# Optimization experiments

Measured on AMD Instinct MI355X. Metric: run time of the kernel, lower is better.

Reference implementation:

```python
import jax, jax.numpy as jnp
import numpy as np

N = 50000
E = 800000
IN_DIM = 128
EMB_DIM = 64
HID = 128
OUT_DIM = 64
VOCAB = 1000
NUM_GRAPHS = 128


def _gat(x, src, dst, W, a_s, a_d, b, n):
    # PyG GATConv, heads=1: h = x @ W (no bias); alpha_e = leaky_relu(a_s.h_src + a_d.h_dst, 0.2)
    h = x @ W                                  # [n, C]
    as_n = h @ a_s                             # [n]
    ad_n = h @ a_d                             # [n]
    logit = jax.nn.leaky_relu(as_n[src] + ad_n[dst], negative_slope=0.2)  # [E']
    # segment softmax over destination node
    m = jax.ops.segment_max(logit, dst, num_segments=n)
    e = jnp.exp(logit - m[dst])
    s = jax.ops.segment_sum(e, dst, num_segments=n)
    coef = e / s[dst]                          # [E']
    out = jax.ops.segment_sum(h[src] * coef[:, None], dst, num_segments=n)
    return out + b


def setup_inputs() -> dict:
    key = jax.random.key(0)
    ks = jax.random.split(key, 20)
    inp = {
        "x": jax.random.normal(ks[0], (N, IN_DIM), dtype=jnp.float32),
        "node_index": jax.random.randint(ks[1], (N,), 0, VOCAB),
        "edge_index": jax.random.randint(ks[2], (2, E), 0, N),
        "batch": jnp.sort(jax.random.randint(ks[3], (N,), 0, NUM_GRAPHS)),
        "emb": jax.random.normal(ks[4], (VOCAB, EMB_DIM), dtype=jnp.float32) * 0.1,
        "W1": jax.random.normal(ks[5], (IN_DIM + EMB_DIM, HID), dtype=jnp.float32) * 0.05,
        "a1s": jax.random.normal(ks[6], (HID,), dtype=jnp.float32) * 0.1,
        "a1d": jax.random.normal(ks[7], (HID,), dtype=jnp.float32) * 0.1,
        "b1": jnp.zeros((HID,), dtype=jnp.float32),
        "W2": jax.random.normal(ks[8], (HID, HID), dtype=jnp.float32) * 0.05,
        "a2s": jax.random.normal(ks[9], (HID,), dtype=jnp.float32) * 0.1,
        "a2d": jax.random.normal(ks[10], (HID,), dtype=jnp.float32) * 0.1,
        "b2": jnp.zeros((HID,), dtype=jnp.float32),
        "W3": jax.random.normal(ks[11], (HID, HID), dtype=jnp.float32) * 0.05,
        "a3s": jax.random.normal(ks[12], (HID,), dtype=jnp.float32) * 0.1,
        "a3d": jax.random.normal(ks[13], (HID,), dtype=jnp.float32) * 0.1,
        "b3": jnp.zeros((HID,), dtype=jnp.float32),
        "fcW": jax.random.normal(ks[14], (HID, OUT_DIM), dtype=jnp.float32) * 0.05,
        "fcb": jnp.zeros((OUT_DIM,), dtype=jnp.float32),
    }
    return inp


def reference(x, node_index, edge_index, batch, emb, W1, a1s, a1d, b1,
              W2, a2s, a2d, b2, W3, a3s, a3d, b3, fcW, fcb):
    n = x.shape[0]
    # embedding lookup + L2 normalize features, then concat
    ev = emb[node_index]                       # [N, EMB_DIM]
    norms = jnp.linalg.norm(x, axis=1, keepdims=True)
    norms = jnp.where(norms == 0, 1e-8, norms)
    h = jnp.concatenate([x / norms, ev], axis=1)  # [N, IN+EMB]
    # add self loops (PyG GATConv default add_self_loops=True)
    loop = jnp.arange(n)
    src = jnp.concatenate([edge_index[0], loop])
    dst = jnp.concatenate([edge_index[1], loop])
    h = jax.nn.gelu(_gat(h, src, dst, W1, a1s, a1d, b1, n))
    h = jax.nn.gelu(_gat(h, src, dst, W2, a2s, a2d, b2, n))
    h = jax.nn.gelu(_gat(h, src, dst, W3, a3s, a3d, b3, n))
    # global_add_pool over graphs
    g = jax.ops.segment_sum(h, batch, num_segments=NUM_GRAPHS)  # [G, HID]
    out = g @ fcW + fcb
    return jax.nn.leaky_relu(out, negative_slope=0.01)
```

## Files before the change

kernel.cpp:

```cpp
#include <hip/hip_runtime.h>

#define N_NODES 50000
#define N_EDGES 800000
#define IN_DIM 128
#define EMB_DIM 64
#define HID 128
#define OUT_DIM 64
#define NUM_GRAPHS 128
#define E_TOT (N_EDGES + N_NODES)
#define K1 (IN_DIM + EMB_DIM)
#define NB 391
#define EPT 16
#define EPB (256 * EPT)

typedef __attribute__((ext_vector_type(8))) short bf16x8;
typedef __attribute__((ext_vector_type(4))) float f32x4;

__device__ __forceinline__ float gelu_f(float x) {
    float x3 = x * x * x;
    return 0.5f * x * (1.0f + tanhf(0.7978845608028654f * (x + 0.044715f * x3)));
}
__device__ __forceinline__ float lrelu02(float x) { return x > 0.f ? x : 0.2f * x; }
__device__ __forceinline__ float rl_f(float v, int j) {
    return __int_as_float(__builtin_amdgcn_readlane(__float_as_int(v), j));
}
__device__ __forceinline__ unsigned short f2bf(float f) {
    unsigned u = __float_as_uint(f);
    unsigned r = (u + 0x7fffu + ((u >> 16) & 1u)) >> 16;
    return (unsigned short)r;
}
__device__ __forceinline__ unsigned pk2bf(float a, float b) {
    return (unsigned)f2bf(a) | ((unsigned)f2bf(b) << 16);
}

__global__ __launch_bounds__(256) void k_zero(int* __restrict__ bcnt, int* __restrict__ bfill) {
    int t = blockIdx.x * 256 + threadIdx.x;
    if (t < NB) { bcnt[t] = 0; bfill[t] = 0; }
}

__global__ __launch_bounds__(128) void k_prepW3(const float* __restrict__ W1, unsigned short* __restrict__ Wt1,
                                                const float* __restrict__ W2, unsigned short* __restrict__ Wt2,
                                                const float* __restrict__ W3, unsigned short* __restrict__ Wt3) {
    int b = blockIdx.x;
    int c = threadIdx.x;
    if (b < K1) {
        Wt1[(size_t)c * (K1 + 8) + b] = f2bf(W1[(size_t)b * HID + c]);
    } else if (b < K1 + HID) {
        int k = b - K1;
        Wt2[(size_t)c * (HID + 8) + k] = f2bf(W2[(size_t)k * HID + c]);
    } else {
        int k = b - K1 - HID;
        Wt3[(size_t)c * (HID + 8) + k] = f2bf(W3[(size_t)k * HID + c]);
    }
}

__global__ __launch_bounds__(256) void k_prepA(const float* __restrict__ x, const int* __restrict__ nidx,
                                               const float* __restrict__ emb, unsigned* __restrict__ Abu) {
    int lane = threadIdx.x & 63;
    int node = (blockIdx.x * 256 + threadIdx.x) >> 6;
    if (node >= N_NODES) return;
    float2 v = ((const float2*)(x + (size_t)node * IN_DIM))[lane];
    float ss = v.x * v.x + v.y * v.y;
#pragma unroll
    for (int o = 32; o; o >>= 1) ss += __shfl_xor(ss, o);
    float nrm = sqrtf(ss);
    if (nrm == 0.f) nrm = 1e-8f;
    float inv = 1.f / nrm;
    unsigned* row = Abu + (size_t)node * (K1 / 2);
    row[lane] = pk2bf(v.x * inv, v.y * inv);
    int nid = __builtin_amdgcn_readfirstlane(nidx[node]);
    if (lane < 32) {
        float2 e = ((const float2*)(emb + (size_t)nid * EMB_DIM))[lane];
        row[64 + lane] = pk2bf(e.x, e.y);
    }
}

__global__ __launch_bounds__(256) void k_bhist(const int* __restrict__ dst, int* __restrict__ bcnt) {
    __shared__ int h[NB];
    for (int i = threadIdx.x; i < NB; i += 256) h[i] = 0;
    __syncthreads();
    for (int e = blockIdx.x * 256 + threadIdx.x; e < N_EDGES; e += gridDim.x * 256)
        atomicAdd(&h[dst[e] >> 7], 1);
    __syncthreads();
    for (int i = threadIdx.x; i < NB; i += 256)
        if (h[i]) atomicAdd(&bcnt[i], h[i]);
}

__global__ __launch_bounds__(512) void k_bscan(const int* __restrict__ bcnt, int* __restrict__ boff,
                                               int* __restrict__ rowptr) {
    __shared__ int sh[512];
    int t = threadIdx.x;
    int v = (t < NB) ? bcnt[t] : 0;
    sh[t] = v;
    __syncthreads();
    for (int o = 1; o < 512; o <<= 1) {
        int u = (t >= o) ? sh[t - o] : 0;
        __syncthreads();
        sh[t] += u;
        __syncthreads();
    }
    if (t < NB) boff[t] = sh[t] - v;
    if (t == NB - 1) boff[NB] = sh[t];
    if (t == 0) rowptr[N_NODES] = E_TOT;
}

__global__ __launch_bounds__(256) void k_passA(const int* __restrict__ src, const int* __restrict__ dst,
                                               const int* __restrict__ boff, int* __restrict__ bfill,
                                               unsigned* __restrict__ barr) {
    __shared__ int h[NB];
    __shared__ int base[NB];
    for (int i = threadIdx.x; i < NB; i += 256) h[i] = 0;
    __syncthreads();
    int e0 = blockIdx.x * EPB;
    int tag[EPT];
#pragma unroll
    for (int i = 0; i < EPT; i++) {
        int e = e0 + i * 256 + threadIdx.x;
        tag[i] = -1;
        if (e < N_EDGES) {
            int b = dst[e] >> 7;
            int r = atomicAdd(&h[b], 1);
            tag[i] = (b << 12) | r;
        }
    }
    __syncthreads();
    for (int i = threadIdx.x; i < NB; i += 256)
        base[i] = h[i] ? atomicAdd(&bfill[i], h[i]) : 0;
    __syncthreads();
#pragma unroll
    for (int i = 0; i < EPT; i++) {
        if (tag[i] >= 0) {
            int e = e0 + i * 256 + threadIdx.x;
            int b = tag[i] >> 12, r = tag[i] & 0xfff;
            unsigned s = (unsigned)src[e];
            unsigned dl = (unsigned)(dst[e] & 127);
            barr[boff[b] + base[b] + r] = s | (dl << 16);
        }
    }
}

__global__ __launch_bounds__(256) void k_passB(const unsigned* __restrict__ barr, const int* __restrict__ boff,
                                               int* __restrict__ rowptr, int* __restrict__ csr) {
    __shared__ int dcnt[128];
    __shared__ int dsum[128];
    __shared__ int locOff[128];
    int b = blockIdx.x;
    int t = threadIdx.x;
    int n0 = b << 7;
    int cnt = min(128, N_NODES - n0);
    int eb = boff[b], ee = boff[b + 1];
    if (t < 128) dcnt[t] = 0;
    __syncthreads();
    for (int i = eb + t; i < ee; i += 256) atomicAdd(&dcnt[barr[i] >> 16], 1);
    __syncthreads();
    int v = 0;
    if (t < 128) {
        v = (t < cnt) ? dcnt[t] + 1 : 0;
        dsum[t] = v;
    }
    __syncthreads();
    for (int o = 1; o < 128; o <<= 1) {
        int u = (t >= o && t < 128) ? dsum[t - o] : 0;
        __syncthreads();
        if (t < 128) dsum[t] += u;
        __syncthreads();
    }
    int csrBase = eb + n0;
    if (t < 128) {
        locOff[t] = dsum[t] - v;
        dcnt[t] = 0;
    }
    if (t < cnt) {
        int loc = dsum[t] - v;
        rowptr[n0 + t] = csrBase + loc;
        csr[csrBase + loc] = n0 + t;
    }
    __syncthreads();
    for (int i = eb + t; i < ee; i += 256) {
        unsigned vv = barr[i];
        int dl = vv >> 16;
        int s = (int)(vv & 0xffffu);
        int k = atomicAdd(&dcnt[dl], 1);
        csr[csrBase + locOff[dl] + 1 + k] = s;
    }
}

template <int K>
__global__ __launch_bounds__(256) void k_mgemm(const unsigned short* __restrict__ Abf,
                                               const unsigned short* __restrict__ WtP,
                                               const float* __restrict__ a_s, const float* __restrict__ a_d,
                                               unsigned short* __restrict__ Hbf,
                                               float* __restrict__ asn, float* __restrict__ adn) {
    constexpr int KP = K + 8;
    constexpr int NK = K / 32;
    __shared__ __align__(16) unsigned short Wl[128 * KP];
    {
        const uint4* gsrc = (const uint4*)WtP;
        uint4* ldst = (uint4*)Wl;
        const int nchunk = 128 * KP * 2 / 16;
        for (int i = threadIdx.x; i < nchunk; i += 256) ldst[i] = gsrc[i];
    }
    int lane = threadIdx.x & 63;
    int wv = threadIdx.x >> 6;
    int rowbase = blockIdx.x * 64 + wv * 16;
    if (rowbase >= N_NODES) { __syncthreads(); return; }
    int l15 = lane & 15, quad = lane >> 4;

    const unsigned short* Abase = Abf + (size_t)(rowbase + l15) * K + quad * 8;
    bf16x8 afr[NK];
#pragma unroll
    for (int i = 0; i < NK; i++) afr[i] = *(const bf16x8*)(Abase + i * 32);

    __syncthreads();

    f32x4 acc[8];
#pragma unroll
    for (int t = 0; t < 8; t++) acc[t] = (f32x4){0.f, 0.f, 0.f, 0.f};
#pragma unroll
    for (int i = 0; i < NK; i++) {
#pragma unroll
        for (int t = 0; t < 8; t++) {
            bf16x8 bf = *(const bf16x8*)(&Wl[(t * 16 + l15) * KP + i * 32 + quad * 8]);
            acc[t] = __builtin_amdgcn_mfma_f32_16x16x32_bf16(afr[i], bf, acc[t], 0, 0, 0);
        }
    }
    float asc[8], adc[8];
#pragma unroll
    for (int t = 0; t < 8; t++) { asc[t] = a_s[t * 16 + l15]; adc[t] = a_d[t * 16 + l15]; }
#pragma unroll
    for (int r = 0; r < 4; r++) {
        int row = rowbase + quad * 4 + r;
        float ps = 0.f, pd = 0.f;
#pragma unroll
        for (int t = 0; t < 8; t++) {
            float v = acc[t][r];
            Hbf[(size_t)row * HID + t * 16 + l15] = f2bf(v);
            ps = fmaf(v, asc[t], ps);
            pd = fmaf(v, adc[t], pd);
        }
#pragma unroll
        for (int o = 1; o < 16; o <<= 1) {
            ps += __shfl_xor(ps, o);
            pd += __shfl_xor(pd, o);
        }
        if (l15 == 0) { asn[row] = ps; adn[row] = pd; }
    }
}

template <bool OUT32>
__global__ __launch_bounds__(256) void k_aggr(const int* __restrict__ rowptr, const int* __restrict__ csr,
                                              const float* __restrict__ asn, const float* __restrict__ adn,
                                              const unsigned short* __restrict__ hbf,
                                              const float* __restrict__ bias, void* __restrict__ outp) {
    __shared__ float sh_e[4][64];
    __shared__ int sh_s[4][64];
    int lane = threadIdx.x & 63;
    int w = threadIdx.x >> 6;
    int node = blockIdx.x * 4 + w;
    if (node >= N_NODES) return;
    int st = rowptr[node], en = rowptr[node + 1];
    int deg = en - st;
    float ad = adn[node];
    const unsigned* hu = (const unsigned*)hbf;
    float2 acc = make_float2(0.f, 0.f);

    if (deg <= 64) {
        int s = 0;
        float l = -1e30f;
        if (lane < deg) {
            s = csr[st + lane];
            l = lrelu02(asn[s] + ad);
        }
        float m = l;
#pragma unroll
        for (int o = 32; o; o >>= 1) m = fmaxf(m, __shfl_xor(m, o));
        float e = (lane < deg) ? __expf(l - m) : 0.f;
        float ssum = e;
#pragma unroll
        for (int o = 32; o; o >>= 1) ssum += __shfl_xor(ssum, o);
        float coef = e / ssum;
        int j = 0;
        for (; j + 8 <= deg; j += 8) {
            int si[8];
            float ci[8];
            unsigned vi[8];
#pragma unroll
            for (int q = 0; q < 8; q++) {
                si[q] = __builtin_amdgcn_readlane(s, j + q);
                ci[q] = rl_f(coef, j + q);
            }
#pragma unroll
            for (int q = 0; q < 8; q++) vi[q] = hu[(size_t)si[q] * 64 + lane];
#pragma unroll
            for (int q = 0; q < 8; q++) {
                acc.x = fmaf(ci[q], __int_as_float(vi[q] << 16), acc.x);
                acc.y = fmaf(ci[q], __int_as_float(vi[q] & 0xffff0000u), acc.y);
            }
        }
        for (; j + 4 <= deg; j += 4) {
            int s0 = __builtin_amdgcn_readlane(s, j);
            int s1 = __builtin_amdgcn_readlane(s, j + 1);
            int s2 = __builtin_amdgcn_readlane(s, j + 2);
            int s3 = __builtin_amdgcn_readlane(s, j + 3);
            float c0 = rl_f(coef, j), c1 = rl_f(coef, j + 1);
            float c2 = rl_f(coef, j + 2), c3 = rl_f(coef, j + 3);
            unsigned v0 = hu[(size_t)s0 * 64 + lane];
            unsigned v1 = hu[(size_t)s1 * 64 + lane];
            unsigned v2 = hu[(size_t)s2 * 64 + lane];
            unsigned v3 = hu[(size_t)s3 * 64 + lane];
            acc.x = fmaf(c0, __int_as_float(v0 << 16), acc.x);
            acc.y = fmaf(c0, __int_as_float(v0 & 0xffff0000u), acc.y);
            acc.x = fmaf(c1, __int_as_float(v1 << 16), acc.x);
            acc.y = fmaf(c1, __int_as_float(v1 & 0xffff0000u), acc.y);
            acc.x = fmaf(c2, __int_as_float(v2 << 16), acc.x);
            acc.y = fmaf(c2, __int_as_float(v2 & 0xffff0000u), acc.y);
            acc.x = fmaf(c3, __int_as_float(v3 << 16), acc.x);
            acc.y = fmaf(c3, __int_as_float(v3 & 0xffff0000u), acc.y);
        }
        for (; j < deg; j++) {
            int s0 = __builtin_amdgcn_readlane(s, j);
            float c0 = rl_f(coef, j);
            unsigned v0 = hu[(size_t)s0 * 64 + lane];
            acc.x = fmaf(c0, __int_as_float(v0 << 16), acc.x);
            acc.y = fmaf(c0, __int_as_float(v0 & 0xffff0000u), acc.y);
        }
    } else {
        float m = -1e30f;
        for (int i = st + lane; i < en; i += 64) {
            float l = lrelu02(asn[csr[i]] + ad);
            m = fmaxf(m, l);
        }
#pragma unroll
        for (int o = 32; o; o >>= 1) m = fmaxf(m, __shfl_xor(m, o));
        float ssum = 0.f;
        for (int i = st + lane; i < en; i += 64) {
            float l = lrelu02(asn[csr[i]] + ad);
            ssum += __expf(l - m);
        }
#pragma unroll
        for (int o = 32; o; o >>= 1) ssum += __shfl_xor(ssum, o);
        float inv = 1.f / ssum;
        for (int base = st; base < en; base += 64) {
            int cnt = min(64, en - base);
            if (lane < cnt) {
                int sx = csr[base + lane];
                float l = lrelu02(asn[sx] + ad);
                sh_e[w][lane] = __expf(l - m) * inv;
                sh_s[w][lane] = sx;
            }
            for (int j = 0; j < cnt; j++) {
                float c = sh_e[w][j];
                int sx = sh_s[w][j];
                unsigned v0 = hu[(size_t)sx * 64 + lane];
                acc.x = fmaf(c, __int_as_float(v0 << 16), acc.x);
                acc.y = fmaf(c, __int_as_float(v0 & 0xffff0000u), acc.y);
            }
        }
    }
    float2 b = ((const float2*)bias)[lane];
    float rx = gelu_f(acc.x + b.x);
    float ry = gelu_f(acc.y + b.y);
    if constexpr (OUT32) {
        ((float2*)outp)[(size_t)node * 64 + lane] = make_float2(rx, ry);
    } else {
        ((unsigned*)outp)[(size_t)node * 64 + lane] = pk2bf(rx, ry);
    }
}

__global__ __launch_bounds__(256) void k_poolfc(const float* __restrict__ h, const int* __restrict__ batch,
                                                const float* __restrict__ fcW, const float* __restrict__ fcb,
                                                float* __restrict__ out) {
    __shared__ float gv[HID];
    __shared__ float tmp[256];
    int g = blockIdx.x;
    int st, en;
    {
        int lo = 0, hi = N_NODES;
        while (lo < hi) { int mid = (lo + hi) >> 1; if (batch[mid] < g) lo = mid + 1; else hi = mid; }
        st = lo;
        lo = st; hi = N_NODES;
        while (lo < hi) { int mid = (lo + hi) >> 1; if (batch[mid] < g + 1) lo = mid + 1; else hi = mid; }
        en = lo;
    }
    int c = threadIdx.x & 127;
    int half = threadIdx.x >> 7;
    float acc = 0.f;
#pragma unroll 4
    for (int n = st + half; n < en; n += 2) acc += h[(size_t)n * HID + c];
    tmp[threadIdx.x] = acc;
    __syncthreads();
    if (threadIdx.x < HID) gv[threadIdx.x] = tmp[threadIdx.x] + tmp[threadIdx.x + 128];
    __syncthreads();
    if (threadIdx.x < OUT_DIM) {
        float a = fcb[threadIdx.x];
#pragma unroll 4
        for (int k = 0; k < HID; k++) a = fmaf(gv[k], fcW[k * OUT_DIM + threadIdx.x], a);
        out[g * OUT_DIM + threadIdx.x] = a > 0.f ? a : 0.01f * a;
    }
}

extern "C" void kernel_launch(void* const* d_in, const int* in_sizes, int n_in,
                              void* d_out, int out_size, void* d_ws, size_t ws_size,
                              hipStream_t stream) {
    const float* x    = (const float*)d_in[0];
    const int* nidx   = (const int*)d_in[1];
    const int* ei     = (const int*)d_in[2];
    const int* batch  = (const int*)d_in[3];
    const float* emb  = (const float*)d_in[4];
    const float* W1   = (const float*)d_in[5];
    const float* a1s  = (const float*)d_in[6];
    const float* a1d  = (const float*)d_in[7];
    const float* b1   = (const float*)d_in[8];
    const float* W2   = (const float*)d_in[9];
    const float* a2s  = (const float*)d_in[10];
    const float* a2d  = (const float*)d_in[11];
    const float* b2   = (const float*)d_in[12];
    const float* W3   = (const float*)d_in[13];
    const float* a3s  = (const float*)d_in[14];
    const float* a3d  = (const float*)d_in[15];
    const float* b3   = (const float*)d_in[16];
    const float* fcW  = (const float*)d_in[17];
    const float* fcb  = (const float*)d_in[18];
    float* out = (float*)d_out;
    const int* srcA = ei;
    const int* dstA = ei + N_EDGES;

    char* w = (char*)d_ws;
    auto alloc = [&](size_t bytes) -> char* {
        char* p = w;
        w += (bytes + 511) & ~(size_t)511;
        return p;
    };
    char* region0 = alloc((size_t)N_NODES * HID * 4);
    unsigned* Abu = (unsigned*)region0;
    float* h3f    = (float*)region0;
    unsigned short* hLin = (unsigned short*)alloc((size_t)N_NODES * HID * 2);
    unsigned short* hAct = (unsigned short*)alloc((size_t)N_NODES * HID * 2);
    float* asn   = (float*)alloc((size_t)N_NODES * 4);
    float* adn   = (float*)alloc((size_t)N_NODES * 4);
    int* rowptr  = (int*)alloc((size_t)(N_NODES + 1) * 4);
    int* bcnt    = (int*)alloc((size_t)NB * 4);
    int* boff    = (int*)alloc((size_t)(NB + 1) * 4);
    int* bfill   = (int*)alloc((size_t)NB * 4);
    unsigned* barr = (unsigned*)alloc((size_t)N_EDGES * 4);
    int* csr     = (int*)alloc((size_t)E_TOT * 4);
    unsigned short* Wt1 = (unsigned short*)alloc((size_t)HID * (K1 + 8) * 2);
    unsigned short* Wt2 = (unsigned short*)alloc((size_t)HID * (HID + 8) * 2);
    unsigned short* Wt3 = (unsigned short*)alloc((size_t)HID * (HID + 8) * 2);

    k_zero<<<(NB + 255) / 256, 256, 0, stream>>>(bcnt, bfill);
    k_prepW3<<<K1 + 2 * HID, 128, 0, stream>>>(W1, Wt1, W2, Wt2, W3, Wt3);
    k_prepA<<<(N_NODES + 3) / 4, 256, 0, stream>>>(x, nidx, emb, Abu);

    k_bhist<<<512, 256, 0, stream>>>(dstA, bcnt);
    k_bscan<<<1, 512, 0, stream>>>(bcnt, boff, rowptr);
    k_passA<<<(N_EDGES + EPB - 1) / EPB, 256, 0, stream>>>(srcA, dstA, boff, bfill, barr);
    k_passB<<<NB, 256, 0, stream>>>(barr, boff, rowptr, csr);

    int gemmBlocks = (N_NODES + 63) / 64;
    int aggrBlocks = (N_NODES + 3) / 4;

    k_mgemm<K1><<<gemmBlocks, 256, 0, stream>>>((const unsigned short*)Abu, Wt1, a1s, a1d, hLin, asn, adn);
    k_aggr<false><<<aggrBlocks, 256, 0, stream>>>(rowptr, csr, asn, adn, hLin, b1, hAct);
    k_mgemm<HID><<<gemmBlocks, 256, 0, stream>>>(hAct, Wt2, a2s, a2d, hLin, asn, adn);
    k_aggr<false><<<aggrBlocks, 256, 0, stream>>>(rowptr, csr, asn, adn, hLin, b2, hAct);
    k_mgemm<HID><<<gemmBlocks, 256, 0, stream>>>(hAct, Wt3, a3s, a3d, hLin, asn, adn);
    k_aggr<true><<<aggrBlocks, 256, 0, stream>>>(rowptr, csr, asn, adn, hLin, b3, h3f);

    k_poolfc<<<NUM_GRAPHS, 256, 0, stream>>>(h3f, batch, fcW, fcb, out);
}
```

Measured before the change: 334.3 us.

## Fuse all stages into one cooperative persistent kernel with grid syncs

Replaces the sequence of about thirteen kernel launches with a single cooperative persistent kernel whose grid-stride phases are separated by grid.sync(), and keeps a multi-launch fallback. The GEMM phase no longer stages the weight matrix in shared memory and instead reads bf16 weight fragments straight from global memory, and the weight transposes drop their padding. The aim is to remove launch gaps and tail effects between the many small phases. In exchange, the persistent grid is capped by occupancy at 4 blocks per CU under the launch bounds, the grid-wide barriers add their own cost, and uncached weight loads may slow the GEMMs.

```diff
diff --git a/kernel.cpp b/kernel.cpp
--- a/kernel.cpp
+++ b/kernel.cpp
@@ -1,4 +1,6 @@
 #include <hip/hip_runtime.h>
+#include <hip/hip_cooperative_groups.h>
+namespace cg = cooperative_groups;
 
 #define N_NODES 50000
 #define N_EDGES 800000
@@ -10,8 +12,11 @@
 #define E_TOT (N_EDGES + N_NODES)
 #define K1 (IN_DIM + EMB_DIM)
 #define NB 391
+#define EPB 4096
+#define NCHUNK ((N_EDGES + EPB - 1) / EPB)
 #define EPT 16
-#define EPB (256 * EPT)
+#define NGRP 12500
+#define NRG 782
 
 typedef __attribute__((ext_vector_type(8))) short bf16x8;
 typedef __attribute__((ext_vector_type(4))) float f32x4;
@@ -33,397 +38,443 @@
     return (unsigned)f2bf(a) | ((unsigned)f2bf(b) << 16);
 }
 
-__global__ __launch_bounds__(256) void k_zero(int* __restrict__ bcnt, int* __restrict__ bfill) {
-    int t = blockIdx.x * 256 + threadIdx.x;
-    if (t < NB) { bcnt[t] = 0; bfill[t] = 0; }
-}
-
-__global__ __launch_bounds__(128) void k_prepW3(const float* __restrict__ W1, unsigned short* __restrict__ Wt1,
-                                                const float* __restrict__ W2, unsigned short* __restrict__ Wt2,
-                                                const float* __restrict__ W3, unsigned short* __restrict__ Wt3) {
-    int b = blockIdx.x;
-    int c = threadIdx.x;
-    if (b < K1) {
-        Wt1[(size_t)c * (K1 + 8) + b] = f2bf(W1[(size_t)b * HID + c]);
-    } else if (b < K1 + HID) {
-        int k = b - K1;
-        Wt2[(size_t)c * (HID + 8) + k] = f2bf(W2[(size_t)k * HID + c]);
-    } else {
-        int k = b - K1 - HID;
-        Wt3[(size_t)c * (HID + 8) + k] = f2bf(W3[(size_t)k * HID + c]);
-    }
-}
-
-__global__ __launch_bounds__(256) void k_prepA(const float* __restrict__ x, const int* __restrict__ nidx,
-                                               const float* __restrict__ emb, unsigned* __restrict__ Abu) {
-    int lane = threadIdx.x & 63;
-    int node = (blockIdx.x * 256 + threadIdx.x) >> 6;
-    if (node >= N_NODES) return;
-    float2 v = ((const float2*)(x + (size_t)node * IN_DIM))[lane];
-    float ss = v.x * v.x + v.y * v.y;
-#pragma unroll
-    for (int o = 32; o; o >>= 1) ss += __shfl_xor(ss, o);
-    float nrm = sqrtf(ss);
-    if (nrm == 0.f) nrm = 1e-8f;
-    float inv = 1.f / nrm;
-    unsigned* row = Abu + (size_t)node * (K1 / 2);
-    row[lane] = pk2bf(v.x * inv, v.y * inv);
-    int nid = __builtin_amdgcn_readfirstlane(nidx[node]);
-    if (lane < 32) {
-        float2 e = ((const float2*)(emb + (size_t)nid * EMB_DIM))[lane];
-        row[64 + lane] = pk2bf(e.x, e.y);
-    }
-}
-
-__global__ __launch_bounds__(256) void k_bhist(const int* __restrict__ dst, int* __restrict__ bcnt) {
+struct MegaArgs {
+    const float* x; const int* nidx; const int* src; const int* dst; const int* batch;
+    const float* emb;
+    const float* W1; const float* a1s; const float* a1d; const float* b1;
+    const float* W2; const float* a2s; const float* a2d; const float* b2;
+    const float* W3; const float* a3s; const float* a3d; const float* b3;
+    const float* fcW; const float* fcb;
+    float* out;
+    unsigned* Abu; float* h3f;
+    unsigned short* hLin; unsigned short* hAct;
+    float* asn; float* adn;
+    int* rowptr; int* bcnt; int* boff; int* bfill;
+    unsigned* barr; int* csr;
+    unsigned short* Wt1; unsigned short* Wt2; unsigned short* Wt3;
+};
+
+
+__device__ void phase_p0(const MegaArgs& A) {
+    const int tid = threadIdx.x, bid = blockIdx.x;
+    const int lane = tid & 63, wv = tid >> 6;
+    const int gtid = bid * 256 + tid;
+    const int nthr = gridDim.x * 256;
+    for (int i = gtid; i < NB; i += nthr) { A.bcnt[i] = 0; A.bfill[i] = 0; }
+    for (int id = gtid; id < 128 * K1; id += nthr) {
+        int c = id / K1, k = id - c * K1;
+        A.Wt1[c * K1 + k] = f2bf(A.W1[(size_t)k * HID + c]);
+    }
+    for (int id = gtid; id < 128 * 128; id += nthr) {
+        int c = id >> 7, k = id & 127;
+        A.Wt2[c * HID + k] = f2bf(A.W2[(size_t)k * HID + c]);
+        A.Wt3[c * HID + k] = f2bf(A.W3[(size_t)k * HID + c]);
+    }
+    for (int g4 = bid; g4 < NGRP; g4 += gridDim.x) {
+        int node = g4 * 4 + wv;
+        if (node >= N_NODES) continue;
+        float2 v = ((const float2*)(A.x + (size_t)node * IN_DIM))[lane];
+        float ss = v.x * v.x + v.y * v.y;
+#pragma unroll
+        for (int o = 32; o; o >>= 1) ss += __shfl_xor(ss, o);
+        float nrm = sqrtf(ss);
+        if (nrm == 0.f) nrm = 1e-8f;
+        float inv = 1.f / nrm;
+        unsigned* row = A.Abu + (size_t)node * (K1 / 2);
+        row[lane] = pk2bf(v.x * inv, v.y * inv);
+        int nid = __builtin_amdgcn_readfirstlane(A.nidx[node]);
+        if (lane < 32) {
+            float2 e = ((const float2*)(A.emb + (size_t)nid * EMB_DIM))[lane];
+            row[64 + lane] = pk2bf(e.x, e.y);
+        }
+    }
+}
+
+__device__ void phase_bhist(const MegaArgs& A, int* h) {
+    const int tid = threadIdx.x;
+    for (int c = blockIdx.x; c < NCHUNK; c += gridDim.x) {
+        for (int i = tid; i < NB; i += 256) h[i] = 0;
+        __syncthreads();
+        int e0 = c * EPB, e1 = min(e0 + EPB, N_EDGES);
+        for (int e = e0 + tid; e < e1; e += 256) atomicAdd(&h[A.dst[e] >> 7], 1);
+        __syncthreads();
+        for (int i = tid; i < NB; i += 256)
+            if (h[i]) atomicAdd(&A.bcnt[i], h[i]);
+        __syncthreads();
+    }
+}
+
+__device__ void phase_bscan(const MegaArgs& A) {
+    const int tid = threadIdx.x;
+    const int lane = tid & 63;
+    if (blockIdx.x == 0 && (tid >> 6) == 0) {
+        int run = 0;
+        for (int c = 0; c < 7; c++) {
+            int i = c * 64 + lane;
+            int v = (i < NB) ? A.bcnt[i] : 0;
+            int s = v;
+#pragma unroll
+            for (int o = 1; o < 64; o <<= 1) {
+                int u = __shfl_up(s, o);
+                if (lane >= o) s += u;
+            }
+            if (i < NB) A.boff[i] = run + s - v;
+            run += __shfl(s, 63);
+        }
+        if (lane == 0) { A.boff[NB] = N_EDGES; A.rowptr[N_NODES] = E_TOT; }
+    }
+}
+
+__device__ void phase_passA(const MegaArgs& A, int* h, int* base) {
+    const int tid = threadIdx.x;
+    for (int c = blockIdx.x; c < NCHUNK; c += gridDim.x) {
+        for (int i = tid; i < NB; i += 256) h[i] = 0;
+        __syncthreads();
+        int e0 = c * EPB;
+        int tag[EPT];
+#pragma unroll
+        for (int i = 0; i < EPT; i++) {
+            int e = e0 + i * 256 + tid;
+            tag[i] = -1;
+            if (e < N_EDGES) {
+                int b = A.dst[e] >> 7;
+                int r = atomicAdd(&h[b], 1);
+                tag[i] = (b << 12) | r;
+            }
+        }
+        __syncthreads();
+        for (int i = tid; i < NB; i += 256)
+            base[i] = h[i] ? atomicAdd(&A.bfill[i], h[i]) : 0;
+        __syncthreads();
+#pragma unroll
+        for (int i = 0; i < EPT; i++) {
+            if (tag[i] >= 0) {
+                int e = e0 + i * 256 + tid;
+                int b = tag[i] >> 12, r = tag[i] & 0xfff;
+                A.barr[A.boff[b] + base[b] + r] =
+                    (unsigned)A.src[e] | ((unsigned)(A.dst[e] & 127) << 16);
+            }
+        }
+        __syncthreads();
+    }
+}
+
+__device__ void phase_passB(const MegaArgs& A, int* dcnt, int* dsum, int* locOff) {
+    const int tid = threadIdx.x;
+    for (int b = blockIdx.x; b < NB; b += gridDim.x) {
+        int n0 = b << 7;
+        int cnt = min(128, N_NODES - n0);
+        int eb = A.boff[b], ee = A.boff[b + 1];
+        if (tid < 128) dcnt[tid] = 0;
+        __syncthreads();
+        for (int i = eb + tid; i < ee; i += 256) atomicAdd(&dcnt[A.barr[i] >> 16], 1);
+        __syncthreads();
+        int v = 0;
+        if (tid < 128) {
+            v = (tid < cnt) ? dcnt[tid] + 1 : 0;
+            dsum[tid] = v;
+        }
+        __syncthreads();
+        for (int o = 1; o < 128; o <<= 1) {
+            int u = (tid >= o && tid < 128) ? dsum[tid - o] : 0;
+            __syncthreads();
+            if (tid < 128) dsum[tid] += u;
+            __syncthreads();
+        }
+        int csrBase = eb + n0;
+        if (tid < 128) {
+            locOff[tid] = dsum[tid] - v;
+            dcnt[tid] = 0;
+        }
+        if (tid < cnt) {
+            int loc = dsum[tid] - v;
+            A.rowptr[n0 + tid] = csrBase + loc;
+            A.csr[csrBase + loc] = n0 + tid;
+        }
+        __syncthreads();
+        for (int i = eb + tid; i < ee; i += 256) {
+            unsigned vv = A.barr[i];
+            int dl = vv >> 16;
+            int s = (int)(vv & 0xffffu);
+            int k = atomicAdd(&dcnt[dl], 1);
+            A.csr[csrBase + locOff[dl] + 1 + k] = s;
+        }
+        __syncthreads();
+    }
+}
+
+template <int K>
+__device__ void phase_mgemm(const unsigned short* __restrict__ Abf, const unsigned short* __restrict__ Wt,
+                            const float* __restrict__ a_s, const float* __restrict__ a_d,
+                            unsigned short* __restrict__ Hbf, float* __restrict__ asn,
+                            float* __restrict__ adn) {
+    const int lane = threadIdx.x & 63;
+    const int wv = threadIdx.x >> 6;
+    const int l15 = lane & 15, quad = lane >> 4;
+    constexpr int NK = K / 32;
+    for (int rg = blockIdx.x; rg < NRG; rg += gridDim.x) {
+        int rowbase = rg * 64 + wv * 16;
+        if (rowbase >= N_NODES) continue;
+        const unsigned short* Abase = Abf + (size_t)(rowbase + l15) * K + quad * 8;
+        bf16x8 afr[NK];
+#pragma unroll
+        for (int i = 0; i < NK; i++) afr[i] = *(const bf16x8*)(Abase + i * 32);
+        f32x4 acc[8];
+#pragma unroll
+        for (int t = 0; t < 8; t++) acc[t] = (f32x4){0.f, 0.f, 0.f, 0.f};
+#pragma unroll
+        for (int i = 0; i < NK; i++) {
+#pragma unroll
+            for (int t = 0; t < 8; t++) {
+                bf16x8 bf = *(const bf16x8*)(Wt + (size_t)(t * 16 + l15) * K + i * 32 + quad * 8);
+                acc[t] = __builtin_amdgcn_mfma_f32_16x16x32_bf16(afr[i], bf, acc[t], 0, 0, 0);
+            }
+        }
+        float asc[8], adc[8];
+#pragma unroll
+        for (int t = 0; t < 8; t++) { asc[t] = a_s[t * 16 + l15]; adc[t] = a_d[t * 16 + l15]; }
+#pragma unroll
+        for (int r = 0; r < 4; r++) {
+            int row = rowbase + quad * 4 + r;
+            float ps = 0.f, pd = 0.f;
+#pragma unroll
+            for (int t = 0; t < 8; t++) {
+                float v = acc[t][r];
+                Hbf[(size_t)row * HID + t * 16 + l15] = f2bf(v);
+                ps = fmaf(v, asc[t], ps);
+                pd = fmaf(v, adc[t], pd);
+            }
+#pragma unroll
+            for (int o = 1; o < 16; o <<= 1) {
+                ps += __shfl_xor(ps, o);
+                pd += __shfl_xor(pd, o);
+            }
+            if (l15 == 0) { asn[row] = ps; adn[row] = pd; }
+        }
+    }
+}
+
+template <bool OUT32>
+__device__ void phase_aggr(const MegaArgs& A, const unsigned short* __restrict__ hbf,
+                           const float* __restrict__ bias, void* __restrict__ outp, char* smem) {
+    float* sh_e = (float*)smem;
+    int* sh_s = (int*)(smem + 1024);
+    const int lane = threadIdx.x & 63;
+    const int w = threadIdx.x >> 6;
+    const unsigned* hu = (const unsigned*)hbf;
+    const int* rowptr = A.rowptr;
+    const int* csr = A.csr;
+    const float* asn = A.asn;
+    const float* adn = A.adn;
+    for (int ng = blockIdx.x; ng < NGRP; ng += gridDim.x) {
+        int node = ng * 4 + w;
+        if (node >= N_NODES) continue;
+        int st = rowptr[node], en = rowptr[node + 1];
+        int deg = en - st;
+        float ad = adn[node];
+        float2 acc = make_float2(0.f, 0.f);
+        if (deg <= 64) {
+            int s = 0;
+            float l = -1e30f;
+            if (lane < deg) {
+                s = csr[st + lane];
+                l = lrelu02(asn[s] + ad);
+            }
+            float m = l;
+#pragma unroll
+            for (int o = 32; o; o >>= 1) m = fmaxf(m, __shfl_xor(m, o));
+            float e = (lane < deg) ? __expf(l - m) : 0.f;
+            float ssum = e;
+#pragma unroll
+            for (int o = 32; o; o >>= 1) ssum += __shfl_xor(ssum, o);
+            float coef = e / ssum;
+            int j = 0;
+            for (; j + 8 <= deg; j += 8) {
+                int si[8]; float ci[8]; unsigned vi[8];
+#pragma unroll
+                for (int q = 0; q < 8; q++) {
+                    si[q] = __builtin_amdgcn_readlane(s, j + q);
+                    ci[q] = rl_f(coef, j + q);
+                }
+#pragma unroll
+                for (int q = 0; q < 8; q++) vi[q] = hu[(size_t)si[q] * 64 + lane];
+#pragma unroll
+                for (int q = 0; q < 8; q++) {
+                    acc.x = fmaf(ci[q], __int_as_float(vi[q] << 16), acc.x);
+                    acc.y = fmaf(ci[q], __int_as_float(vi[q] & 0xffff0000u), acc.y);
+                }
+            }
+            for (; j < deg; j++) {
+                int s0 = __builtin_amdgcn_readlane(s, j);
+                float c0 = rl_f(coef, j);
+                unsigned v0 = hu[(size_t)s0 * 64 + lane];
+                acc.x = fmaf(c0, __int_as_float(v0 << 16), acc.x);
+                acc.y = fmaf(c0, __int_as_float(v0 & 0xffff0000u), acc.y);
+            }
+        } else {
+            float m = -1e30f;
+            for (int i = st + lane; i < en; i += 64) {
+                float l = lrelu02(asn[csr[i]] + ad);
+                m = fmaxf(m, l);
+            }
+#pragma unroll
+            for (int o = 32; o; o >>= 1) m = fmaxf(m, __shfl_xor(m, o));
+            float ssum = 0.f;
+            for (int i = st + lane; i < en; i += 64) {
+                float l = lrelu02(asn[csr[i]] + ad);
+                ssum += __expf(l - m);
+            }
+#pragma unroll
+            for (int o = 32; o; o >>= 1) ssum += __shfl_xor(ssum, o);
+            float inv = 1.f / ssum;
+            for (int base = st; base < en; base += 64) {
+                int cnt = min(64, en - base);
+                if (lane < cnt) {
+                    int sx = csr[base + lane];
+                    float l = lrelu02(asn[sx] + ad);
+                    sh_e[w * 64 + lane] = __expf(l - m) * inv;
+                    sh_s[w * 64 + lane] = sx;
+                }
+                for (int j = 0; j < cnt; j++) {
+                    float c = sh_e[w * 64 + j];
+                    int sx = sh_s[w * 64 + j];
+                    unsigned v0 = hu[(size_t)sx * 64 + lane];
+                    acc.x = fmaf(c, __int_as_float(v0 << 16), acc.x);
+                    acc.y = fmaf(c, __int_as_float(v0 & 0xffff0000u), acc.y);
+                }
+            }
+        }
+        float2 b = ((const float2*)bias)[lane];
+        float rx = gelu_f(acc.x + b.x);
+        float ry = gelu_f(acc.y + b.y);
+        if constexpr (OUT32) {
+            ((float2*)outp)[(size_t)node * 64 + lane] = make_float2(rx, ry);
+        } else {
+            ((unsigned*)outp)[(size_t)node * 64 + lane] = pk2bf(rx, ry);
+        }
+    }
+}
+
+__device__ void phase_poolfc(const MegaArgs& A, char* smem) {
+    float* gv = (float*)smem;
+    float* tmp = (float*)(smem + 512);
+    const int tid = threadIdx.x;
+    for (int g = blockIdx.x; g < NUM_GRAPHS; g += gridDim.x) {
+        int st, en;
+        {
+            int lo = 0, hi = N_NODES;
+            while (lo < hi) { int mid = (lo + hi) >> 1; if (A.batch[mid] < g) lo = mid + 1; else hi = mid; }
+            st = lo;
+            lo = st; hi = N_NODES;
+            while (lo < hi) { int mid = (lo + hi) >> 1; if (A.batch[mid] < g + 1) lo = mid + 1; else hi = mid; }
+            en = lo;
+        }
+        int c = tid & 127;
+        int half = tid >> 7;
+        float acc = 0.f;
+        for (int n = st + half; n < en; n += 2) acc += A.h3f[(size_t)n * HID + c];
+        tmp[tid] = acc;
+        __syncthreads();
+        if (tid < HID) gv[tid] = tmp[tid] + tmp[tid + 128];
+        __syncthreads();
+        if (tid < OUT_DIM) {
+            float a = A.fcb[tid];
+#pragma unroll 4
+            for (int k = 0; k < HID; k++) a = fmaf(gv[k], A.fcW[k * OUT_DIM + tid], a);
+            A.out[g * OUT_DIM + tid] = a > 0.f ? a : 0.01f * a;
+        }
+        __syncthreads();
+    }
+}
+
+__global__ __launch_bounds__(256, 4) void k_mega(MegaArgs A) {
+    __shared__ __align__(16) char smem[4608];
+    cg::grid_group grid = cg::this_grid();
+    phase_p0(A);
+    grid.sync();
+    phase_bhist(A, (int*)smem);
+    grid.sync();
+    phase_bscan(A);
+    grid.sync();
+    phase_passA(A, (int*)smem, (int*)(smem + 1568));
+    grid.sync();
+    phase_passB(A, (int*)smem, (int*)(smem + 512), (int*)(smem + 1024));
+    grid.sync();
+    phase_mgemm<K1>((const unsigned short*)A.Abu, A.Wt1, A.a1s, A.a1d, A.hLin, A.asn, A.adn);
+    grid.sync();
+    phase_aggr<false>(A, A.hLin, A.b1, A.hAct, smem);
+    grid.sync();
+    phase_mgemm<HID>(A.hAct, A.Wt2, A.a2s, A.a2d, A.hLin, A.asn, A.adn);
+    grid.sync();
+    phase_aggr<false>(A, A.hLin, A.b2, A.hAct, smem);
+    grid.sync();
+    phase_mgemm<HID>(A.hAct, A.Wt3, A.a3s, A.a3d, A.hLin, A.asn, A.adn);
+    grid.sync();
+    phase_aggr<true>(A, A.hLin, A.b3, A.h3f, smem);
+    grid.sync();
+    phase_poolfc(A, smem);
+}
+
+__global__ __launch_bounds__(256) void kf_p0(MegaArgs A) { phase_p0(A); }
+__global__ __launch_bounds__(256) void kf_bhist(MegaArgs A) {
     __shared__ int h[NB];
-    for (int i = threadIdx.x; i < NB; i += 256) h[i] = 0;
-    __syncthreads();
-    for (int e = blockIdx.x * 256 + threadIdx.x; e < N_EDGES; e += gridDim.x * 256)
-        atomicAdd(&h[dst[e] >> 7], 1);
-    __syncthreads();
-    for (int i = threadIdx.x; i < NB; i += 256)
-        if (h[i]) atomicAdd(&bcnt[i], h[i]);
-}
-
-__global__ __launch_bounds__(512) void k_bscan(const int* __restrict__ bcnt, int* __restrict__ boff,
-                                               int* __restrict__ rowptr) {
-    __shared__ int sh[512];
-    int t = threadIdx.x;
-    int v = (t < NB) ? bcnt[t] : 0;
-    sh[t] = v;
-    __syncthreads();
-    for (int o = 1; o < 512; o <<= 1) {
-        int u = (t >= o) ? sh[t - o] : 0;
-        __syncthreads();
-        sh[t] += u;
-        __syncthreads();
-    }
-    if (t < NB) boff[t] = sh[t] - v;
-    if (t == NB - 1) boff[NB] = sh[t];
-    if (t == 0) rowptr[N_NODES] = E_TOT;
-}
-
-__global__ __launch_bounds__(256) void k_passA(const int* __restrict__ src, const int* __restrict__ dst,
-                                               const int* __restrict__ boff, int* __restrict__ bfill,
-                                               unsigned* __restrict__ barr) {
+    phase_bhist(A, h);
+}
+__global__ __launch_bounds__(256) void kf_bscan(MegaArgs A) { phase_bscan(A); }
+__global__ __launch_bounds__(256) void kf_passA(MegaArgs A) {
     __shared__ int h[NB];
     __shared__ int base[NB];
-    for (int i = threadIdx.x; i < NB; i += 256) h[i] = 0;
-    __syncthreads();
-    int e0 = blockIdx.x * EPB;
-    int tag[EPT];
-#pragma unroll
-    for (int i = 0; i < EPT; i++) {
-        int e = e0 + i * 256 + threadIdx.x;
-        tag[i] = -1;
-        if (e < N_EDGES) {
-            int b = dst[e] >> 7;
-            int r = atomicAdd(&h[b], 1);
-            tag[i] = (b << 12) | r;
-        }
-    }
-    __syncthreads();
-    for (int i = threadIdx.x; i < NB; i += 256)
-        base[i] = h[i] ? atomicAdd(&bfill[i], h[i]) : 0;
-    __syncthreads();
-#pragma unroll
-    for (int i = 0; i < EPT; i++) {
-        if (tag[i] >= 0) {
-            int e = e0 + i * 256 + threadIdx.x;
-            int b = tag[i] >> 12, r = tag[i] & 0xfff;
-            unsigned s = (unsigned)src[e];
-            unsigned dl = (unsigned)(dst[e] & 127);
-            barr[boff[b] + base[b] + r] = s | (dl << 16);
-        }
-    }
-}
-
-__global__ __launch_bounds__(256) void k_passB(const unsigned* __restrict__ barr, const int* __restrict__ boff,
-                                               int* __restrict__ rowptr, int* __restrict__ csr) {
-    __shared__ int dcnt[128];
-    __shared__ int dsum[128];
-    __shared__ int locOff[128];
-    int b = blockIdx.x;
-    int t = threadIdx.x;
-    int n0 = b << 7;
-    int cnt = min(128, N_NODES - n0);
-    int eb = boff[b], ee = boff[b + 1];
-    if (t < 128) dcnt[t] = 0;
-    __syncthreads();
-    for (int i = eb + t; i < ee; i += 256) atomicAdd(&dcnt[barr[i] >> 16], 1);
-    __syncthreads();
-    int v = 0;
-    if (t < 128) {
-        v = (t < cnt) ? dcnt[t] + 1 : 0;
-        dsum[t] = v;
-    }
-    __syncthreads();
-    for (int o = 1; o < 128; o <<= 1) {
-        int u = (t >= o && t < 128) ? dsum[t - o] : 0;
-        __syncthreads();
-        if (t < 128) dsum[t] += u;
-        __syncthreads();
-    }
-    int csrBase = eb + n0;
-    if (t < 128) {
-        locOff[t] = dsum[t] - v;
-        dcnt[t] = 0;
-    }
-    if (t < cnt) {
-        int loc = dsum[t] - v;
-        rowptr[n0 + t] = csrBase + loc;
-        csr[csrBase + loc] = n0 + t;
-    }
-    __syncthreads();
-    for (int i = eb + t; i < ee; i += 256) {
-        unsigned vv = barr[i];
-        int dl = vv >> 16;
-        int s = (int)(vv & 0xffffu);
-        int k = atomicAdd(&dcnt[dl], 1);
-        csr[csrBase + locOff[dl] + 1 + k] = s;
-    }
-}
-
-template <int K>
-__global__ __launch_bounds__(256) void k_mgemm(const unsigned short* __restrict__ Abf,
-                                               const unsigned short* __restrict__ WtP,
-                                               const float* __restrict__ a_s, const float* __restrict__ a_d,
-                                               unsigned short* __restrict__ Hbf,
-                                               float* __restrict__ asn, float* __restrict__ adn) {
-    constexpr int KP = K + 8;
-    constexpr int NK = K / 32;
-    __shared__ __align__(16) unsigned short Wl[128 * KP];
-    {
-        const uint4* gsrc = (const uint4*)WtP;
-        uint4* ldst = (uint4*)Wl;
-        const int nchunk = 128 * KP * 2 / 16;
-        for (int i = threadIdx.x; i < nchunk; i += 256) ldst[i] = gsrc[i];
-    }
-    int lane = threadIdx.x & 63;
-    int wv = threadIdx.x >> 6;
-    int rowbase = blockIdx.x * 64 + wv * 16;
-    if (rowbase >= N_NODES) { __syncthreads(); return; }
-    int l15 = lane & 15, quad = lane >> 4;
-
-    const unsigned short* Abase = Abf + (size_t)(rowbase + l15) * K + quad * 8;
-    bf16x8 afr[NK];
-#pragma unroll
-    for (int i = 0; i < NK; i++) afr[i] = *(const bf16x8*)(Abase + i * 32);
-
-    __syncthreads();
-
-    f32x4 acc[8];
-#pragma unroll
-    for (int t = 0; t < 8; t++) acc[t] = (f32x4){0.f, 0.f, 0.f, 0.f};
-#pragma unroll
-    for (int i = 0; i < NK; i++) {
-#pragma unroll
-        for (int t = 0; t < 8; t++) {
-            bf16x8 bf = *(const bf16x8*)(&Wl[(t * 16 + l15) * KP + i * 32 + quad * 8]);
-            acc[t] = __builtin_amdgcn_mfma_f32_16x16x32_bf16(afr[i], bf, acc[t], 0, 0, 0);
-        }
-    }
-    float asc[8], adc[8];
-#pragma unroll
-    for (int t = 0; t < 8; t++) { asc[t] = a_s[t * 16 + l15]; adc[t] = a_d[t * 16 + l15]; }
-#pragma unroll
-    for (int r = 0; r < 4; r++) {
-        int row = rowbase + quad * 4 + r;
-        float ps = 0.f, pd = 0.f;
-#pragma unroll
-        for (int t = 0; t < 8; t++) {
-            float v = acc[t][r];
-            Hbf[(size_t)row * HID + t * 16 + l15] = f2bf(v);
-            ps = fmaf(v, asc[t], ps);
-            pd = fmaf(v, adc[t], pd);
-        }
-#pragma unroll
-        for (int o = 1; o < 16; o <<= 1) {
-            ps += __shfl_xor(ps, o);
-            pd += __shfl_xor(pd, o);
-        }
-        if (l15 == 0) { asn[row] = ps; adn[row] = pd; }
-    }
-}
-
-template <bool OUT32>
-__global__ __launch_bounds__(256) void k_aggr(const int* __restrict__ rowptr, const int* __restrict__ csr,
-                                              const float* __restrict__ asn, const float* __restrict__ adn,
-                                              const unsigned short* __restrict__ hbf,
-                                              const float* __restrict__ bias, void* __restrict__ outp) {
-    __shared__ float sh_e[4][64];
-    __shared__ int sh_s[4][64];
-    int lane = threadIdx.x & 63;
-    int w = threadIdx.x >> 6;
-    int node = blockIdx.x * 4 + w;
-    if (node >= N_NODES) return;
-    int st = rowptr[node], en = rowptr[node + 1];
-    int deg = en - st;
-    float ad = adn[node];
-    const unsigned* hu = (const unsigned*)hbf;
-    float2 acc = make_float2(0.f, 0.f);
-
-    if (deg <= 64) {
-        int s = 0;
-        float l = -1e30f;
-        if (lane < deg) {
-            s = csr[st + lane];
-            l = lrelu02(asn[s] + ad);
-        }
-        float m = l;
-#pragma unroll
-        for (int o = 32; o; o >>= 1) m = fmaxf(m, __shfl_xor(m, o));
-        float e = (lane < deg) ? __expf(l - m) : 0.f;
-        float ssum = e;
-#pragma unroll
-        for (int o = 32; o; o >>= 1) ssum += __shfl_xor(ssum, o);
-        float coef = e / ssum;
-        int j = 0;
-        for (; j + 8 <= deg; j += 8) {
-            int si[8];
-            float ci[8];
-            unsigned vi[8];
-#pragma unroll
-            for (int q = 0; q < 8; q++) {
-                si[q] = __builtin_amdgcn_readlane(s, j + q);
-                ci[q] = rl_f(coef, j + q);
-            }
-#pragma unroll
-            for (int q = 0; q < 8; q++) vi[q] = hu[(size_t)si[q] * 64 + lane];
-#pragma unroll
-            for (int q = 0; q < 8; q++) {
-                acc.x = fmaf(ci[q], __int_as_float(vi[q] << 16), acc.x);
-                acc.y = fmaf(ci[q], __int_as_float(vi[q] & 0xffff0000u), acc.y);
-            }
-        }
-        for (; j + 4 <= deg; j += 4) {
-            int s0 = __builtin_amdgcn_readlane(s, j);
-            int s1 = __builtin_amdgcn_readlane(s, j + 1);
-            int s2 = __builtin_amdgcn_readlane(s, j + 2);
-            int s3 = __builtin_amdgcn_readlane(s, j + 3);
-            float c0 = rl_f(coef, j), c1 = rl_f(coef, j + 1);
-            float c2 = rl_f(coef, j + 2), c3 = rl_f(coef, j + 3);
-            unsigned v0 = hu[(size_t)s0 * 64 + lane];
-            unsigned v1 = hu[(size_t)s1 * 64 + lane];
-            unsigned v2 = hu[(size_t)s2 * 64 + lane];
-            unsigned v3 = hu[(size_t)s3 * 64 + lane];
-            acc.x = fmaf(c0, __int_as_float(v0 << 16), acc.x);
-            acc.y = fmaf(c0, __int_as_float(v0 & 0xffff0000u), acc.y);
-            acc.x = fmaf(c1, __int_as_float(v1 << 16), acc.x);
-            acc.y = fmaf(c1, __int_as_float(v1 & 0xffff0000u), acc.y);
-            acc.x = fmaf(c2, __int_as_float(v2 << 16), acc.x);
-            acc.y = fmaf(c2, __int_as_float(v2 & 0xffff0000u), acc.y);
-            acc.x = fmaf(c3, __int_as_float(v3 << 16), acc.x);
-            acc.y = fmaf(c3, __int_as_float(v3 & 0xffff0000u), acc.y);
-        }
-        for (; j < deg; j++) {
-            int s0 = __builtin_amdgcn_readlane(s, j);
-            float c0 = rl_f(coef, j);
-            unsigned v0 = hu[(size_t)s0 * 64 + lane];
-            acc.x = fmaf(c0, __int_as_float(v0 << 16), acc.x);
-            acc.y = fmaf(c0, __int_as_float(v0 & 0xffff0000u), acc.y);
-        }
-    } else {
-        float m = -1e30f;
-        for (int i = st + lane; i < en; i += 64) {
-            float l = lrelu02(asn[csr[i]] + ad);
-            m = fmaxf(m, l);
-        }
-#pragma unroll
-        for (int o = 32; o; o >>= 1) m = fmaxf(m, __shfl_xor(m, o));
-        float ssum = 0.f;
-        for (int i = st + lane; i < en; i += 64) {
-            float l = lrelu02(asn[csr[i]] + ad);
-            ssum += __expf(l - m);
-        }
-#pragma unroll
-        for (int o = 32; o; o >>= 1) ssum += __shfl_xor(ssum, o);
-        float inv = 1.f / ssum;
-        for (int base = st; base < en; base += 64) {
-            int cnt = min(64, en - base);
-            if (lane < cnt) {
-                int sx = csr[base + lane];
-                float l = lrelu02(asn[sx] + ad);
-                sh_e[w][lane] = __expf(l - m) * inv;
-                sh_s[w][lane] = sx;
-            }
-            for (int j = 0; j < cnt; j++) {
-                float c = sh_e[w][j];
-                int sx = sh_s[w][j];
-                unsigned v0 = hu[(size_t)sx * 64 + lane];
-                acc.x = fmaf(c, __int_as_float(v0 << 16), acc.x);
-                acc.y = fmaf(c, __int_as_float(v0 & 0xffff0000u), acc.y);
-            }
-        }
-    }
-    float2 b = ((const float2*)bias)[lane];
-    float rx = gelu_f(acc.x + b.x);
-    float ry = gelu_f(acc.y + b.y);
-    if constexpr (OUT32) {
-        ((float2*)outp)[(size_t)node * 64 + lane] = make_float2(rx, ry);
-    } else {
-        ((unsigned*)outp)[(size_t)node * 64 + lane] = pk2bf(rx, ry);
-    }
-}
-
-__global__ __launch_bounds__(256) void k_poolfc(const float* __restrict__ h, const int* __restrict__ batch,
-                                                const float* __restrict__ fcW, const float* __restrict__ fcb,
-                                                float* __restrict__ out) {
-    __shared__ float gv[HID];
-    __shared__ float tmp[256];
-    int g = blockIdx.x;
-    int st, en;
-    {
-        int lo = 0, hi = N_NODES;
-        while (lo < hi) { int mid = (lo + hi) >> 1; if (batch[mid] < g) lo = mid + 1; else hi = mid; }
-        st = lo;
-        lo = st; hi = N_NODES;
-        while (lo < hi) { int mid = (lo + hi) >> 1; if (batch[mid] < g + 1) lo = mid + 1; else hi = mid; }
-        en = lo;
-    }
-    int c = threadIdx.x & 127;
-    int half = threadIdx.x >> 7;
-    float acc = 0.f;
-#pragma unroll 4
-    for (int n = st + half; n < en; n += 2) acc += h[(size_t)n * HID + c];
-    tmp[threadIdx.x] = acc;
-    __syncthreads();
-    if (threadIdx.x < HID) gv[threadIdx.x] = tmp[threadIdx.x] + tmp[threadIdx.x + 128];
-    __syncthreads();
-    if (threadIdx.x < OUT_DIM) {
-        float a = fcb[threadIdx.x];
-#pragma unroll 4
-        for (int k = 0; k < HID; k++) a = fmaf(gv[k], fcW[k * OUT_DIM + threadIdx.x], a);
-        out[g * OUT_DIM + threadIdx.x] = a > 0.f ? a : 0.01f * a;
-    }
+    phase_passA(A, h, base);
+}
+__global__ __launch_bounds__(256) void kf_passB(MegaArgs A) {
+    __shared__ int dcnt[128], dsum[128], locOff[128];
+    phase_passB(A, dcnt, dsum, locOff);
+}
+__global__ __launch_bounds__(256) void kf_mgemm1(MegaArgs A) {
+    phase_mgemm<K1>((const unsigned short*)A.Abu, A.Wt1, A.a1s, A.a1d, A.hLin, A.asn, A.adn);
+}
+__global__ __launch_bounds__(256) void kf_mgemm2(MegaArgs A) {
+    phase_mgemm<HID>(A.hAct, A.Wt2, A.a2s, A.a2d, A.hLin, A.asn, A.adn);
+}
+__global__ __launch_bounds__(256) void kf_mgemm3(MegaArgs A) {
+    phase_mgemm<HID>(A.hAct, A.Wt3, A.a3s, A.a3d, A.hLin, A.asn, A.adn);
+}
+__global__ __launch_bounds__(256) void kf_aggr1(MegaArgs A) {
+    __shared__ __align__(16) char smem[2048];
+    phase_aggr<false>(A, A.hLin, A.b1, A.hAct, smem);
+}
+__global__ __launch_bounds__(256) void kf_aggr2(MegaArgs A) {
+    __shared__ __align__(16) char smem[2048];
+    phase_aggr<false>(A, A.hLin, A.b2, A.hAct, smem);
+}
+__global__ __launch_bounds__(256) void kf_aggr3(MegaArgs A) {
+    __shared__ __align__(16) char smem[2048];
+    phase_aggr<true>(A, A.hLin, A.b3, A.h3f, smem);
+}
+__global__ __launch_bounds__(256) void kf_poolfc(MegaArgs A) {
+    __shared__ __align__(16) char smem[1536];
+    phase_poolfc(A, smem);
 }
 
 extern "C" void kernel_launch(void* const* d_in, const int* in_sizes, int n_in,
                               void* d_out, int out_size, void* d_ws, size_t ws_size,
                               hipStream_t stream) {
-    const float* x    = (const float*)d_in[0];
-    const int* nidx   = (const int*)d_in[1];
-    const int* ei     = (const int*)d_in[2];
-    const int* batch  = (const int*)d_in[3];
-    const float* emb  = (const float*)d_in[4];
-    const float* W1   = (const float*)d_in[5];
-    const float* a1s  = (const float*)d_in[6];
-    const float* a1d  = (const float*)d_in[7];
-    const float* b1   = (const float*)d_in[8];
-    const float* W2   = (const float*)d_in[9];
-    const float* a2s  = (const float*)d_in[10];
-    const float* a2d  = (const float*)d_in[11];
-    const float* b2   = (const float*)d_in[12];
-    const float* W3   = (const float*)d_in[13];
-    const float* a3s  = (const float*)d_in[14];
-    const float* a3d  = (const float*)d_in[15];
-    const float* b3   = (const float*)d_in[16];
-    const float* fcW  = (const float*)d_in[17];
-    const float* fcb  = (const float*)d_in[18];
-    float* out = (float*)d_out;
-    const int* srcA = ei;
-    const int* dstA = ei + N_EDGES;
+    MegaArgs a;
+    a.x    = (const float*)d_in[0];
+    a.nidx = (const int*)d_in[1];
+    const int* ei = (const int*)d_in[2];
+    a.src  = ei;
+    a.dst  = ei + N_EDGES;
+    a.batch = (const int*)d_in[3];
+    a.emb  = (const float*)d_in[4];
+    a.W1 = (const float*)d_in[5];  a.a1s = (const float*)d_in[6];
+    a.a1d = (const float*)d_in[7]; a.b1 = (const float*)d_in[8];
+    a.W2 = (const float*)d_in[9];  a.a2s = (const float*)d_in[10];
+    a.a2d = (const float*)d_in[11]; a.b2 = (const float*)d_in[12];
+    a.W3 = (const float*)d_in[13]; a.a3s = (const float*)d_in[14];
+    a.a3d = (const float*)d_in[15]; a.b3 = (const float*)d_in[16];
+    a.fcW = (const float*)d_in[17]; a.fcb = (const float*)d_in[18];
+    a.out = (float*)d_out;
 
     char* w = (char*)d_ws;
     auto alloc = [&](size_t bytes) -> char* {
@@ -432,40 +483,48 @@
         return p;
     };
     char* region0 = alloc((size_t)N_NODES * HID * 4);
-    unsigned* Abu = (unsigned*)region0;
-    float* h3f    = (float*)region0;
-    unsigned short* hLin = (unsigned short*)alloc((size_t)N_NODES * HID * 2);
-    unsigned short* hAct = (unsigned short*)alloc((size_t)N_NODES * HID * 2);
-    float* asn   = (float*)alloc((size_t)N_NODES * 4);
-    float* adn   = (float*)alloc((size_t)N_NODES * 4);
-    int* rowptr  = (int*)alloc((size_t)(N_NODES + 1) * 4);
-    int* bcnt    = (int*)alloc((size_t)NB * 4);
-    int* boff    = (int*)alloc((size_t)(NB + 1) * 4);
-    int* bfill   = (int*)alloc((size_t)NB * 4);
-    unsigned* barr = (unsigned*)alloc((size_t)N_EDGES * 4);
-    int* csr     = (int*)alloc((size_t)E_TOT * 4);
-    unsigned short* Wt1 = (unsigned short*)alloc((size_t)HID * (K1 + 8) * 2);
-    unsigned short* Wt2 = (unsigned short*)alloc((size_t)HID * (HID + 8) * 2);
-    unsigned short* Wt3 = (unsigned short*)alloc((size_t)HID * (HID + 8) * 2);
-
-    k_zero<<<(NB + 255) / 256, 256, 0, stream>>>(bcnt, bfill);
-    k_prepW3<<<K1 + 2 * HID, 128, 0, stream>>>(W1, Wt1, W2, Wt2, W3, Wt3);
-    k_prepA<<<(N_NODES + 3) / 4, 256, 0, stream>>>(x, nidx, emb, Abu);
-
-    k_bhist<<<512, 256, 0, stream>>>(dstA, bcnt);
-    k_bscan<<<1, 512, 0, stream>>>(bcnt, boff, rowptr);
-    k_passA<<<(N_EDGES + EPB - 1) / EPB, 256, 0, stream>>>(srcA, dstA, boff, bfill, barr);
-    k_passB<<<NB, 256, 0, stream>>>(barr, boff, rowptr, csr);
-
-    int gemmBlocks = (N_NODES + 63) / 64;
-    int aggrBlocks = (N_NODES + 3) / 4;
-
-    k_mgemm<K1><<<gemmBlocks, 256, 0, stream>>>((const unsigned short*)Abu, Wt1, a1s, a1d, hLin, asn, adn);
-    k_aggr<false><<<aggrBlocks, 256, 0, stream>>>(rowptr, csr, asn, adn, hLin, b1, hAct);
-    k_mgemm<HID><<<gemmBlocks, 256, 0, stream>>>(hAct, Wt2, a2s, a2d, hLin, asn, adn);
-    k_aggr<false><<<aggrBlocks, 256, 0, stream>>>(rowptr, csr, asn, adn, hLin, b2, hAct);
-    k_mgemm<HID><<<gemmBlocks, 256, 0, stream>>>(hAct, Wt3, a3s, a3d, hLin, asn, adn);
-    k_aggr<true><<<aggrBlocks, 256, 0, stream>>>(rowptr, csr, asn, adn, hLin, b3, h3f);
-
-    k_poolfc<<<NUM_GRAPHS, 256, 0, stream>>>(h3f, batch, fcW, fcb, out);
-}
+    a.Abu = (unsigned*)region0;
+    a.h3f = (float*)region0;
+    a.hLin = (unsigned short*)alloc((size_t)N_NODES * HID * 2);
+    a.hAct = (unsigned short*)alloc((size_t)N_NODES * HID * 2);
+    a.asn = (float*)alloc((size_t)N_NODES * 4);
+    a.adn = (float*)alloc((size_t)N_NODES * 4);
+    a.rowptr = (int*)alloc((size_t)(N_NODES + 1) * 4);
+    a.bcnt = (int*)alloc((size_t)NB * 4);
+    a.boff = (int*)alloc((size_t)(NB + 1) * 4);
+    a.bfill = (int*)alloc((size_t)NB * 4);
+    a.barr = (unsigned*)alloc((size_t)N_EDGES * 4);
+    a.csr = (int*)alloc((size_t)E_TOT * 4);
+    a.Wt1 = (unsigned short*)alloc((size_t)HID * K1 * 2);
+    a.Wt2 = (unsigned short*)alloc((size_t)HID * HID * 2);
+    a.Wt3 = (unsigned short*)alloc((size_t)HID * HID * 2);
+
+    int dev = 0;
+    hipError_t e0 = hipGetDevice(&dev);
+    int numCU = 0;
+    hipError_t e1 = hipDeviceGetAttribute(&numCU, hipDeviceAttributeMultiprocessorCount, dev);
+    int maxB = 0;
+    hipError_t qerr = hipOccupancyMaxActiveBlocksPerMultiprocessor(&maxB, k_mega, 256, 0);
+
+    hipError_t lerr = hipErrorUnknown;
+    if (e0 == hipSuccess && e1 == hipSuccess && qerr == hipSuccess && maxB >= 1 && numCU >= 1) {
+        int grid = maxB * numCU;
+        if (grid > 2048) grid = 2048;
+        void* kp[] = { &a };
+        lerr = hipLaunchCooperativeKernel(k_mega, dim3(grid), dim3(256), kp, 0, stream);
+    }
+    if (lerr != hipSuccess) {
+        kf_p0<<<1024, 256, 0, stream>>>(a);
+        kf_bhist<<<NCHUNK, 256, 0, stream>>>(a);
+        kf_bscan<<<1, 256, 0, stream>>>(a);
+        kf_passA<<<NCHUNK, 256, 0, stream>>>(a);
+        kf_passB<<<NB, 256, 0, stream>>>(a);
+        kf_mgemm1<<<NRG, 256, 0, stream>>>(a);
+        kf_aggr1<<<NGRP, 256, 0, stream>>>(a);
+        kf_mgemm2<<<NRG, 256, 0, stream>>>(a);
+        kf_aggr2<<<NGRP, 256, 0, stream>>>(a);
+        kf_mgemm3<<<NRG, 256, 0, stream>>>(a);
+        kf_aggr3<<<NGRP, 256, 0, stream>>>(a);
+        kf_poolfc<<<NUM_GRAPHS, 256, 0, stream>>>(a);
+    }
+}
```

After: 414.6 us. 24.0% more time.
